# Performance work log

Measured on AMD Instinct MI355X. Metric: run time of the kernel, lower is better.

Reference implementation:

```python
import jax, jax.numpy as jnp
import numpy as np

B, D, K = 4, 128, 512   # batch, node_embedding_dim, num_nodes
ALPHA = 0.2             # LeakyReLU negative slope


def setup_inputs() -> dict:
    key = jax.random.key(0)
    k1, k2, k3, k4 = jax.random.split(key, 4)
    x = jax.random.normal(k1, (B, D, K), dtype=jnp.float32)
    # nn.Linear(2D -> D): store weight as (2D, D) for right-multiplication
    lin_w = jax.random.normal(k2, (2 * D, D), dtype=jnp.float32) * (1.0 / np.sqrt(2 * D))
    lin_b = jax.random.normal(k3, (D,), dtype=jnp.float32) * 0.01
    # attention vector a: (D,) (xavier-uniform in torch; scale-equivalent normal here)
    a = jax.random.normal(k4, (D,), dtype=jnp.float32) * (1.414 * np.sqrt(2.0 / (D + 1)))
    bias_mat = jnp.zeros((K, K), dtype=jnp.float32)  # init zeros per module
    return {"x": x, "lin_w": lin_w, "lin_b": lin_b, "a": a, "bias_mat": bias_mat}


def reference(x, lin_w, lin_b, a, bias_mat):
    # x: (B, D, K) -> transpose to (B, K, D); GATv2 path, residual = identity
    xt = jnp.swapaxes(x, 1, 2)                      # (B, K, D)
    d = xt.shape[-1]
    # lin(concat(v_i, v_j)) == v_i @ W1 + v_j @ W2 + b  (exact split; avoids (B,K,K,2D) concat)
    W1, W2 = lin_w[:d], lin_w[d:]
    left = xt @ W1 + lin_b                          # (B, K, D) -- v_i part (repeating block)
    right = xt @ W2                                 # (B, K, D) -- v_j part (alternating block)
    pre = left[:, :, None, :] + right[:, None, :, :]  # (B, K, K, D)
    h = jnp.where(pre > 0, pre, ALPHA * pre)        # LeakyReLU
    e = jnp.einsum('bijd,d->bij', h, a) + bias_mat  # (B, K, K)
    attn = jax.nn.softmax(e, axis=2)                # softmax over j (dropout p=0)
    agg = jnp.einsum('bij,bjd->bid', attn, xt)      # (B, K, D)
    out = jax.nn.sigmoid(agg) + xt                  # sigmoid + identity residual
    return jnp.swapaxes(out, 1, 2)                  # (B, D, K)
```

## Files before the change

### kernel.cpp

```cpp
#include <hip/hip_runtime.h>

#define B 4
#define D 128
#define K 512
#define TI 4

typedef __fp16 h2v __attribute__((ext_vector_type(2)));

__device__ __forceinline__ unsigned pkrtz(float a, float b) {
  h2v h = __builtin_amdgcn_cvt_pkrtz(a, b);
  union { h2v h; unsigned u; } c; c.h = h; return c.u;
}
__device__ __forceinline__ h2v u2h(unsigned u) {
  union { unsigned u; h2v h; } c; c.u = u; return c.h;
}
__device__ __forceinline__ float fdot2f(h2v a, h2v b, float c) {
#if __has_builtin(__builtin_amdgcn_fdot2)
  return __builtin_amdgcn_fdot2(a, b, c, false);
#else
  return c + (float)a.x * (float)b.x + (float)a.y * (float)b.y;
#endif
}
__device__ __forceinline__ h2v relu2(h2v a) {
#if __has_builtin(__builtin_elementwise_max)
  const h2v z = {(__fp16)0.f, (__fp16)0.f};
  return __builtin_elementwise_max(a, z);
#else
  h2v r;
  r.x = (float)a.x > 0.f ? a.x : (__fp16)0.f;
  r.y = (float)a.y > 0.f ? a.y : (__fp16)0.f;
  return r;
#endif
}

__global__ __launch_bounds__(256) void gat_lr16(
    const float* __restrict__ x, const float* __restrict__ lin_w,
    const float* __restrict__ lin_b, const float* __restrict__ a,
    unsigned* __restrict__ LhT, unsigned* __restrict__ RhT,
    unsigned* __restrict__ XhT) {
  const int j0 = blockIdx.x * 64;
  const int E0 = blockIdx.y * 16;
  const int b = blockIdx.z;
  const int t = threadIdx.x;
  __shared__ float sx[D][64];
  __shared__ float sw1[D][16];
  __shared__ float sw2[D][16];
#pragma unroll
  for (int r = 0; r < 8; ++r) {
    const int fid = t + 256 * r;
    const int row = fid >> 4, c4 = fid & 15;
    *(float4*)&sx[row][4 * c4] =
        *(const float4*)&x[((size_t)b * D + row) * K + j0 + 4 * c4];
  }
#pragma unroll
  for (int r = 0; r < 8; ++r) {
    const int idx = t + 256 * r;
    const int row = idx >> 4, e = idx & 15;
    sw1[row][e] = lin_w[(size_t)row * D + E0 + e];
    sw2[row][e] = lin_w[(size_t)(D + row) * D + E0 + e];
  }
  __syncthreads();
  {
    const int ry = blockIdx.y * 2;
#pragma unroll
    for (int r = ry; r < ry + 2; ++r) {
      const int idx = t + 256 * r;
      const int row = idx >> 5, jc = idx & 31;
      XhT[((size_t)b * D + row) * (K / 2) + (j0 >> 1) + jc] =
          pkrtz(sx[row][2 * jc], sx[row][2 * jc + 1]);
    }
  }
  const int j = t & 63, g = t >> 6;
  float accL[4] = {0.f, 0.f, 0.f, 0.f}, accR[4] = {0.f, 0.f, 0.f, 0.f};
#pragma unroll 8
  for (int c = 0; c < D; ++c) {
    const float xv = sx[c][j];
    const float4 w1 = *(const float4*)&sw1[c][4 * g];
    const float4 w2 = *(const float4*)&sw2[c][4 * g];
    accL[0] = fmaf(xv, w1.x, accL[0]);
    accL[1] = fmaf(xv, w1.y, accL[1]);
    accL[2] = fmaf(xv, w1.z, accL[2]);
    accL[3] = fmaf(xv, w1.w, accL[3]);
    accR[0] = fmaf(xv, w2.x, accR[0]);
    accR[1] = fmaf(xv, w2.y, accR[1]);
    accR[2] = fmaf(xv, w2.z, accR[2]);
    accR[3] = fmaf(xv, w2.w, accR[3]);
  }
  const int e0 = E0 + 4 * g;
#pragma unroll
  for (int u = 0; u < 2; ++u) {
    const int ea = e0 + 2 * u, eb = ea + 1;
    const float uea = 0.8f * fabsf(a[ea]), ueb = 0.8f * fabsf(a[eb]);
    const float La = uea * (accL[2 * u] + lin_b[ea]);
    const float Lb = ueb * (accL[2 * u + 1] + lin_b[eb]);
    const float Ra = uea * accR[2 * u];
    const float Rb = ueb * accR[2 * u + 1];
    const size_t dp = (size_t)(ea >> 1);
    LhT[((size_t)b * (D / 2) + dp) * K + j0 + j] = pkrtz(La, Lb);
    RhT[((size_t)b * (D / 2) + dp) * K + j0 + j] = pkrtz(Ra, Rb);
  }
}

__global__ __launch_bounds__(256) void gat_attn16(
    const float* __restrict__ x, const float* __restrict__ a,
    const float* __restrict__ bias, const unsigned* __restrict__ LhT,
    const unsigned* __restrict__ RhT, const unsigned* __restrict__ XhT,
    float* __restrict__ out) {
  const int i0 = blockIdx.x * TI;
  const int b = blockIdx.y;
  const int t = threadIdx.x;
  __shared__ float sxt[D][TI];
  __shared__ unsigned slh[D / 2][TI];
  __shared__ unsigned ssg[D / 2];
  __shared__ float sSL[TI];
  __shared__ float seT[TI][K];
  __shared__ unsigned sattn16[TI][K / 2];

  {
    int idx = t;
    sxt[idx >> 2][idx & 3] = x[((size_t)b * D + (idx >> 2)) * K + i0 + (idx & 3)];
    idx = t + 256;
    sxt[idx >> 2][idx & 3] = x[((size_t)b * D + (idx >> 2)) * K + i0 + (idx & 3)];
    const int dp = t >> 2, ii = t & 3;
    slh[dp][ii] = LhT[((size_t)b * (D / 2) + dp) * K + i0 + ii];
    if (t < D / 2) {
      const float s0 = (a[2 * t] >= 0.f) ? 1.f : -1.f;
      const float s1 = (a[2 * t + 1] >= 0.f) ? 1.f : -1.f;
      ssg[t] = pkrtz(s0, s1);
    }
  }
  __syncthreads();
  {
    const int ii = t >> 6, dp = t & 63;
    float v = fdot2f(u2h(ssg[dp]), u2h(slh[dp][ii]), 0.f);
#pragma unroll
    for (int off = 32; off > 0; off >>= 1) v += __shfl_xor(v, off, 64);
    if ((t & 63) == 0) sSL[ii] = v;
  }
  __syncthreads();

  {
    const unsigned* rc = RhT + (size_t)b * (D / 2) * K;
    float accA[4] = {0.f, 0.f, 0.f, 0.f}, accB[4] = {0.f, 0.f, 0.f, 0.f};
    float srA = 0.f, srB = 0.f;
#pragma unroll 4
    for (int dp = 0; dp < D / 2; ++dp) {
      const uint2 rr = *(const uint2*)&rc[(size_t)dp * K + 2 * t];
      const uint4 lh4 = *(const uint4*)&slh[dp][0];
      const h2v s2 = u2h(ssg[dp]);
      const h2v rva = u2h(rr.x), rvb = u2h(rr.y);
      srA = fdot2f(s2, rva, srA);
      srB = fdot2f(s2, rvb, srB);
      h2v l;
      l = u2h(lh4.x);
      accA[0] = fdot2f(s2, relu2(l + rva), accA[0]);
      accB[0] = fdot2f(s2, relu2(l + rvb), accB[0]);
      l = u2h(lh4.y);
      accA[1] = fdot2f(s2, relu2(l + rva), accA[1]);
      accB[1] = fdot2f(s2, relu2(l + rvb), accB[1]);
      l = u2h(lh4.z);
      accA[2] = fdot2f(s2, relu2(l + rva), accA[2]);
      accB[2] = fdot2f(s2, relu2(l + rvb), accB[2]);
      l = u2h(lh4.w);
      accA[3] = fdot2f(s2, relu2(l + rva), accA[3]);
      accB[3] = fdot2f(s2, relu2(l + rvb), accB[3]);
    }
#pragma unroll
    for (int ii = 0; ii < TI; ++ii) {
      const float2 bv = *(const float2*)&bias[(size_t)(i0 + ii) * K + 2 * t];
      float2 ev;
      ev.x = accA[ii] + 0.25f * (sSL[ii] + srA) + bv.x;
      ev.y = accB[ii] + 0.25f * (sSL[ii] + srB) + bv.y;
      *(float2*)&seT[ii][2 * t] = ev;
    }
  }
  __syncthreads();

  {
    const int w = t >> 6, lane = t & 63;
    float2 v[4];
    float m = -1e30f;
#pragma unroll
    for (int q = 0; q < 4; ++q) {
      v[q] = *(const float2*)&seT[w][2 * lane + 128 * q];
      m = fmaxf(m, fmaxf(v[q].x, v[q].y));
    }
#pragma unroll
    for (int off = 32; off > 0; off >>= 1) m = fmaxf(m, __shfl_xor(m, off, 64));
    float s = 0.f;
#pragma unroll
    for (int q = 0; q < 4; ++q) {
      v[q].x = __expf(v[q].x - m);
      v[q].y = __expf(v[q].y - m);
      s += v[q].x + v[q].y;
    }
#pragma unroll
    for (int off = 32; off > 0; off >>= 1) s += __shfl_xor(s, off, 64);
    const float inv = 1.f / s;
#pragma unroll
    for (int q = 0; q < 4; ++q)
      sattn16[w][lane + 64 * q] = pkrtz(v[q].x * inv, v[q].y * inv);
  }
  __syncthreads();

  {
    const int jr = t & 15, dg = t >> 4;
    uint4 ar[4][4];
#pragma unroll
    for (int i = 0; i < 4; ++i)
#pragma unroll
      for (int q = 0; q < 4; ++q)
        ar[i][q] = *(const uint4*)&sattn16[i][4 * (jr + 16 * q)];
    const unsigned* xh = XhT + (size_t)b * D * (K / 2);
#pragma unroll 2
    for (int r = 0; r < 8; ++r) {
      const int d = dg * 8 + r;
      float acc[4] = {0.f, 0.f, 0.f, 0.f};
#pragma unroll
      for (int q = 0; q < 4; ++q) {
        const uint4 xp =
            *(const uint4*)&xh[(size_t)d * (K / 2) + 4 * (jr + 16 * q)];
#pragma unroll
        for (int i = 0; i < 4; ++i) {
          acc[i] = fdot2f(u2h(ar[i][q].x), u2h(xp.x), acc[i]);
          acc[i] = fdot2f(u2h(ar[i][q].y), u2h(xp.y), acc[i]);
          acc[i] = fdot2f(u2h(ar[i][q].z), u2h(xp.z), acc[i]);
          acc[i] = fdot2f(u2h(ar[i][q].w), u2h(xp.w), acc[i]);
        }
      }
#pragma unroll
      for (int i = 0; i < 4; ++i) {
        acc[i] += __shfl_xor(acc[i], 1, 64);
        acc[i] += __shfl_xor(acc[i], 2, 64);
        acc[i] += __shfl_xor(acc[i], 4, 64);
        acc[i] += __shfl_xor(acc[i], 8, 64);
      }
      if (jr == 0) {
#pragma unroll
        for (int i = 0; i < 4; ++i) {
          const float sg = 1.f / (1.f + __expf(-acc[i]));
          out[((size_t)b * D + d) * K + i0 + i] = sg + sxt[d][i];
        }
      }
    }
  }
}

#define ALPHA 0.2f
__global__ __launch_bounds__(512) void gat_fused(
    const float* __restrict__ x, const float* __restrict__ lin_w,
    const float* __restrict__ lin_b, const float* __restrict__ a,
    const float* __restrict__ bias, float* __restrict__ out) {
  const int i = blockIdx.x, b = blockIdx.y, t = threadIdx.x;
  __shared__ float sxi[D], sLi[D], sa[D];
  __shared__ float lpart[4 * D];
  __shared__ float xtT[D * 64];
  __shared__ float epars[8 * 64];
  __shared__ float se[K];
  __shared__ float sattn[K], spart[K];
  __shared__ float sred[8];

  if (t < D) {
    sxi[t] = x[((size_t)b * D + t) * K + i];
    sa[t] = a[t];
  }
  __syncthreads();
  {
    const int c = t & (D - 1), q = t >> 7;
    float acc = 0.f;
    const float* W1 = lin_w + c;
#pragma unroll 8
    for (int d = q * 32; d < q * 32 + 32; ++d)
      acc = fmaf(sxi[d], W1[(size_t)d * D], acc);
    lpart[q * D + c] = acc;
  }
  __syncthreads();
  if (t < D)
    sLi[t] = lin_b[t] + lpart[t] + lpart[D + t] + lpart[2 * D + t] +
             lpart[3 * D + t];
  __syncthreads();

  for (int jt = 0; jt < K / 64; ++jt) {
    const int j0 = jt * 64;
    for (int idx = t; idx < D * 64; idx += 512)
      xtT[idx] = x[((size_t)b * D + (idx >> 6)) * K + j0 + (idx & 63)];
    __syncthreads();
    const int jj = t & 63, g = t >> 6, dp0 = g * 16;
    float accv[16];
#pragma unroll
    for (int v = 0; v < 16; ++v) accv[v] = 0.f;
    for (int dc = 0; dc < D; dc += 16) {
      float xv[16];
#pragma unroll
      for (int u = 0; u < 16; ++u) xv[u] = xtT[(dc + u) * 64 + jj];
#pragma unroll
      for (int u = 0; u < 16; ++u) {
        const float* W2r = lin_w + (size_t)(D + dc + u) * D + dp0;
#pragma unroll
        for (int v = 0; v < 16; ++v) accv[v] = fmaf(xv[u], W2r[v], accv[v]);
      }
    }
    float ep = 0.f;
#pragma unroll
    for (int v = 0; v < 16; ++v) {
      const float pre = sLi[dp0 + v] + accv[v];
      ep = fmaf(sa[dp0 + v], pre > 0.f ? pre : ALPHA * pre, ep);
    }
    epars[g * 64 + jj] = ep;
    __syncthreads();
    if (t < 64) {
      float esum = bias[(size_t)i * K + j0 + t];
#pragma unroll
      for (int g2 = 0; g2 < 8; ++g2) esum += epars[g2 * 64 + t];
      se[j0 + t] = esum;
    }
    __syncthreads();
  }

  float e = se[t];
  float m = e;
#pragma unroll
  for (int off = 32; off > 0; off >>= 1) m = fmaxf(m, __shfl_xor(m, off, 64));
  if ((t & 63) == 0) sred[t >> 6] = m;
  __syncthreads();
  m = sred[0];
#pragma unroll
  for (int w = 1; w < 8; ++w) m = fmaxf(m, sred[w]);
  const float ev = __expf(e - m);
  float s = ev;
#pragma unroll
  for (int off = 32; off > 0; off >>= 1) s += __shfl_xor(s, off, 64);
  __syncthreads();
  if ((t & 63) == 0) sred[t >> 6] = s;
  __syncthreads();
  s = 0.f;
#pragma unroll
  for (int w = 0; w < 8; ++w) s += sred[w];
  sattn[t] = ev * (1.f / s);
  __syncthreads();

  const int d = t >> 2, c = t & 3;
  const float4* X4 = (const float4*)(x + ((size_t)b * D + d) * K);
  const float4* A4 = (const float4*)sattn;
  float p = 0.f;
#pragma unroll 4
  for (int q = 0; q < K / 16; ++q) {
    const int idx = c + 4 * q;
    float4 xv = X4[idx], av = A4[idx];
    p = fmaf(av.x, xv.x, p);
    p = fmaf(av.y, xv.y, p);
    p = fmaf(av.z, xv.z, p);
    p = fmaf(av.w, xv.w, p);
  }
  spart[t] = p;
  __syncthreads();
  if (t < D) {
    const float agg =
        spart[4 * t] + spart[4 * t + 1] + spart[4 * t + 2] + spart[4 * t + 3];
    const float sg = 1.f / (1.f + __expf(-agg));
    out[((size_t)b * D + t) * K + i] = sg + sxi[t];
  }
}

extern "C" void kernel_launch(void* const* d_in, const int* in_sizes, int n_in,
                              void* d_out, int out_size, void* d_ws,
                              size_t ws_size, hipStream_t stream) {
  const float* x = (const float*)d_in[0];
  const float* lin_w = (const float*)d_in[1];
  const float* lin_b = (const float*)d_in[2];
  const float* a = (const float*)d_in[3];
  const float* bias = (const float*)d_in[4];
  float* out = (float*)d_out;

  const size_t half_words = (size_t)B * (D / 2) * K;
  const size_t xh_words = (size_t)B * D * (K / 2);
  const size_t need = (2 * half_words + xh_words) * sizeof(unsigned);
  if (ws_size >= need && d_ws != nullptr) {
    unsigned* LhT = (unsigned*)d_ws;
    unsigned* RhT = LhT + half_words;
    unsigned* XhT = RhT + half_words;
    gat_lr16<<<dim3(K / 64, D / 16, B), 256, 0, stream>>>(x, lin_w, lin_b, a,
                                                          LhT, RhT, XhT);
    gat_attn16<<<dim3(K / TI, B), 256, 0, stream>>>(x, a, bias, LhT, RhT, XhT,
                                                    out);
  } else {
    gat_fused<<<dim3(K, B), 512, 0, stream>>>(x, lin_w, lin_b, a, bias, out);
  }
}
```

Baseline: 89.34 us.

## Retile attention kernel to 8 query rows per 512-thread block

The attention kernel now handles 8 query rows per block instead of 4 and runs 512 threads, one key column per thread. Each RhT value and each half-precision x row read in the aggregation step is reused across twice as many rows, roughly halving global reads per output. The aggregation loop now covers 4 d-values per thread group with 8 accumulators each, so register pressure rises. The grid shrinks to 256 blocks, which may leave fewer waves to hide latency on a 256-CU part.

```diff
diff --git a/kernel.cpp b/kernel.cpp
--- a/kernel.cpp
+++ b/kernel.cpp
@@ -3,7 +3,7 @@
 #define B 4
 #define D 128
 #define K 512
-#define TI 4
+#define TI 8
 
 typedef __fp16 h2v __attribute__((ext_vector_type(2)));
 
@@ -101,7 +101,7 @@
   }
 }
 
-__global__ __launch_bounds__(256) void gat_attn16(
+__global__ __launch_bounds__(512, 2) void gat_attn16(
     const float* __restrict__ x, const float* __restrict__ a,
     const float* __restrict__ bias, const unsigned* __restrict__ LhT,
     const unsigned* __restrict__ RhT, const unsigned* __restrict__ XhT,
@@ -118,10 +118,10 @@
 
   {
     int idx = t;
-    sxt[idx >> 2][idx & 3] = x[((size_t)b * D + (idx >> 2)) * K + i0 + (idx & 3)];
-    idx = t + 256;
-    sxt[idx >> 2][idx & 3] = x[((size_t)b * D + (idx >> 2)) * K + i0 + (idx & 3)];
-    const int dp = t >> 2, ii = t & 3;
+    sxt[idx >> 3][idx & 7] = x[((size_t)b * D + (idx >> 3)) * K + i0 + (idx & 7)];
+    idx = t + 512;
+    sxt[idx >> 3][idx & 7] = x[((size_t)b * D + (idx >> 3)) * K + i0 + (idx & 7)];
+    const int dp = t >> 3, ii = t & 7;
     slh[dp][ii] = LhT[((size_t)b * (D / 2) + dp) * K + i0 + ii];
     if (t < D / 2) {
       const float s0 = (a[2 * t] >= 0.f) ? 1.f : -1.f;
@@ -140,39 +140,30 @@
   __syncthreads();
 
   {
-    const unsigned* rc = RhT + (size_t)b * (D / 2) * K;
-    float accA[4] = {0.f, 0.f, 0.f, 0.f}, accB[4] = {0.f, 0.f, 0.f, 0.f};
-    float srA = 0.f, srB = 0.f;
-#pragma unroll 4
+    const unsigned* rc = RhT + (size_t)b * (D / 2) * K + t;
+    float acc[8] = {0.f, 0.f, 0.f, 0.f, 0.f, 0.f, 0.f, 0.f};
+    float sr = 0.f;
+#pragma unroll 8
     for (int dp = 0; dp < D / 2; ++dp) {
-      const uint2 rr = *(const uint2*)&rc[(size_t)dp * K + 2 * t];
-      const uint4 lh4 = *(const uint4*)&slh[dp][0];
+      const unsigned rr = rc[(size_t)dp * K];
+      const uint4 lh4a = *(const uint4*)&slh[dp][0];
+      const uint4 lh4b = *(const uint4*)&slh[dp][4];
       const h2v s2 = u2h(ssg[dp]);
-      const h2v rva = u2h(rr.x), rvb = u2h(rr.y);
-      srA = fdot2f(s2, rva, srA);
-      srB = fdot2f(s2, rvb, srB);
-      h2v l;
-      l = u2h(lh4.x);
-      accA[0] = fdot2f(s2, relu2(l + rva), accA[0]);
-      accB[0] = fdot2f(s2, relu2(l + rvb), accB[0]);
-      l = u2h(lh4.y);
-      accA[1] = fdot2f(s2, relu2(l + rva), accA[1]);
-      accB[1] = fdot2f(s2, relu2(l + rvb), accB[1]);
-      l = u2h(lh4.z);
-      accA[2] = fdot2f(s2, relu2(l + rva), accA[2]);
-      accB[2] = fdot2f(s2, relu2(l + rvb), accB[2]);
-      l = u2h(lh4.w);
-      accA[3] = fdot2f(s2, relu2(l + rva), accA[3]);
-      accB[3] = fdot2f(s2, relu2(l + rvb), accB[3]);
-    }
-#pragma unroll
-    for (int ii = 0; ii < TI; ++ii) {
-      const float2 bv = *(const float2*)&bias[(size_t)(i0 + ii) * K + 2 * t];
-      float2 ev;
-      ev.x = accA[ii] + 0.25f * (sSL[ii] + srA) + bv.x;
-      ev.y = accB[ii] + 0.25f * (sSL[ii] + srB) + bv.y;
-      *(float2*)&seT[ii][2 * t] = ev;
-    }
+      const h2v rv = u2h(rr);
+      sr = fdot2f(s2, rv, sr);
+      acc[0] = fdot2f(s2, relu2(u2h(lh4a.x) + rv), acc[0]);
+      acc[1] = fdot2f(s2, relu2(u2h(lh4a.y) + rv), acc[1]);
+      acc[2] = fdot2f(s2, relu2(u2h(lh4a.z) + rv), acc[2]);
+      acc[3] = fdot2f(s2, relu2(u2h(lh4a.w) + rv), acc[3]);
+      acc[4] = fdot2f(s2, relu2(u2h(lh4b.x) + rv), acc[4]);
+      acc[5] = fdot2f(s2, relu2(u2h(lh4b.y) + rv), acc[5]);
+      acc[6] = fdot2f(s2, relu2(u2h(lh4b.z) + rv), acc[6]);
+      acc[7] = fdot2f(s2, relu2(u2h(lh4b.w) + rv), acc[7]);
+    }
+#pragma unroll
+    for (int ii = 0; ii < TI; ++ii)
+      seT[ii][t] = acc[ii] + 0.25f * (sSL[ii] + sr) +
+                   bias[(size_t)(i0 + ii) * K + t];
   }
   __syncthreads();
 
@@ -205,23 +196,23 @@
 
   {
     const int jr = t & 15, dg = t >> 4;
-    uint4 ar[4][4];
-#pragma unroll
-    for (int i = 0; i < 4; ++i)
+    uint4 ar[8][4];
+#pragma unroll
+    for (int i = 0; i < 8; ++i)
 #pragma unroll
       for (int q = 0; q < 4; ++q)
         ar[i][q] = *(const uint4*)&sattn16[i][4 * (jr + 16 * q)];
     const unsigned* xh = XhT + (size_t)b * D * (K / 2);
 #pragma unroll 2
-    for (int r = 0; r < 8; ++r) {
-      const int d = dg * 8 + r;
-      float acc[4] = {0.f, 0.f, 0.f, 0.f};
+    for (int r = 0; r < 4; ++r) {
+      const int d = dg * 4 + r;
+      float acc[8] = {0.f, 0.f, 0.f, 0.f, 0.f, 0.f, 0.f, 0.f};
 #pragma unroll
       for (int q = 0; q < 4; ++q) {
         const uint4 xp =
             *(const uint4*)&xh[(size_t)d * (K / 2) + 4 * (jr + 16 * q)];
 #pragma unroll
-        for (int i = 0; i < 4; ++i) {
+        for (int i = 0; i < 8; ++i) {
           acc[i] = fdot2f(u2h(ar[i][q].x), u2h(xp.x), acc[i]);
           acc[i] = fdot2f(u2h(ar[i][q].y), u2h(xp.y), acc[i]);
           acc[i] = fdot2f(u2h(ar[i][q].z), u2h(xp.z), acc[i]);
@@ -229,7 +220,7 @@
         }
       }
 #pragma unroll
-      for (int i = 0; i < 4; ++i) {
+      for (int i = 0; i < 8; ++i) {
         acc[i] += __shfl_xor(acc[i], 1, 64);
         acc[i] += __shfl_xor(acc[i], 2, 64);
         acc[i] += __shfl_xor(acc[i], 4, 64);
@@ -237,7 +228,7 @@
       }
       if (jr == 0) {
 #pragma unroll
-        for (int i = 0; i < 4; ++i) {
+        for (int i = 0; i < 8; ++i) {
           const float sg = 1.f / (1.f + __expf(-acc[i]));
           out[((size_t)b * D + d) * K + i0 + i] = sg + sxt[d][i];
         }
@@ -381,7 +372,7 @@
     unsigned* XhT = RhT + half_words;
     gat_lr16<<<dim3(K / 64, D / 16, B), 256, 0, stream>>>(x, lin_w, lin_b, a,
                                                           LhT, RhT, XhT);
-    gat_attn16<<<dim3(K / TI, B), 256, 0, stream>>>(x, a, bias, LhT, RhT, XhT,
+    gat_attn16<<<dim3(K / TI, B), 512, 0, stream>>>(x, a, bias, LhT, RhT, XhT,
                                                     out);
   } else {
     gat_fused<<<dim3(K, B), 512, 0, stream>>>(x, lin_w, lin_b, a, bias, out);
```

New measurement: 85.12 us. -4.7%, faster.
